# Kernel tuning notes

Hardware: AMD Instinct MI355X
Metric: run time of the kernel (lower is better)

## Reference

```python
import jax, jax.numpy as jnp
import numpy as np

HEADS = 16
DIM_HEAD = 64
QUERY_DIM = 1024
INNER = HEADS * DIM_HEAD


def setup_inputs() -> dict:
    key = jax.random.key(0)
    ks = jax.random.split(key, 6)
    b, n = 4, 2048
    s = 0.02
    return {
        "x": jax.random.normal(ks[0], (b, n, QUERY_DIM), dtype=jnp.float32),
        "Wq": jax.random.normal(ks[1], (QUERY_DIM, INNER), dtype=jnp.float32) * s,
        "Wk": jax.random.normal(ks[2], (QUERY_DIM, INNER), dtype=jnp.float32) * s,
        "Wv": jax.random.normal(ks[3], (QUERY_DIM, INNER), dtype=jnp.float32) * s,
        "Wo": jax.random.normal(ks[4], (INNER, QUERY_DIM), dtype=jnp.float32) * s,
        "bo": jax.random.normal(ks[5], (QUERY_DIM,), dtype=jnp.float32) * s,
    }


def reference(x, Wq, Wk, Wv, Wo, bo):
    b, n, _ = x.shape
    scale = DIM_HEAD ** (-0.5)
    # project and split heads: [b, n, inner] -> [b, h, n, d]
    def split(t):
        return t.reshape(b, n, HEADS, DIM_HEAD).transpose(0, 2, 1, 3)
    q = split(x @ Wq)
    k = split(x @ Wk)
    v = split(x @ Wv)
    sim = jnp.einsum('bhid,bhjd->bhij', q, k) * scale  # [b, h, n, n]
    attn = jax.nn.softmax(sim, axis=-1)
    out = jnp.einsum('bhij,bhjd->bhid', attn, v)  # [b, h, n, d]
    out = out.transpose(0, 2, 1, 3).reshape(b, n, INNER)
    return out @ Wo + bo
```

## Files before the change

### kernel.cpp

```cpp
#include <hip/hip_runtime.h>

typedef __attribute__((ext_vector_type(8))) short bf16x8;
typedef __attribute__((ext_vector_type(4))) float f32x4;
typedef __attribute__((ext_vector_type(16))) float f32x16;
typedef __attribute__((ext_vector_type(2))) unsigned u32x2;

__device__ __forceinline__ unsigned short f2b(float f) {
  union { float f; unsigned u; } x; x.f = f;
  unsigned r = x.u + 0x7fffu + ((x.u >> 16) & 1u);
  return (unsigned short)(r >> 16);
}

__device__ __forceinline__ int cvt_pk_bf16(float lo, float hi) {
  int r;
  asm("v_cvt_pk_bf16_f32 %0, %1, %2" : "=v"(r) : "v"(lo), "v"(hi));
  return r;
}

__device__ __forceinline__ float exp2_fast(float x) {
#if __has_builtin(__builtin_amdgcn_exp2f)
  return __builtin_amdgcn_exp2f(x);
#else
  return __expf(x * 0.69314718055994531f);
#endif
}

__device__ __forceinline__ void gl_lds16(const unsigned short* g, unsigned short* l) {
  __builtin_amdgcn_global_load_lds(
      (const __attribute__((address_space(1))) unsigned int*)(unsigned long long)g,
      (__attribute__((address_space(3))) unsigned int*)(unsigned)(unsigned long long)l,
      16, 0, 0);
}

#define MFMA(a, b, c) __builtin_amdgcn_mfma_f32_16x16x32_bf16((a), (b), (c), 0, 0, 0)
#define MFMA32(a, b, c) __builtin_amdgcn_mfma_f32_32x32x16_bf16((a), (b), (c), 0, 0, 0)

__global__ __launch_bounds__(256) void prep(const float* __restrict__ x, unsigned short* __restrict__ xb,
                                            const float* __restrict__ wq, const float* __restrict__ wk,
                                            const float* __restrict__ wv, const float* __restrict__ wo,
                                            unsigned short* __restrict__ tq, unsigned short* __restrict__ tk,
                                            unsigned short* __restrict__ tv, unsigned short* __restrict__ to_) {
  int lin = blockIdx.x;
  int t = threadIdx.x;
  if (lin < 8192) {
    int i = (lin * 256 + t) * 4;
    float4 v = *(const float4*)(x + i);
    ushort4 o;
    o.x = f2b(v.x); o.y = f2b(v.y); o.z = f2b(v.z); o.w = f2b(v.w);
    *(ushort4*)(xb + i) = o;
    return;
  }
  int blk = lin - 8192;
  int z = blk >> 8;
  int rem = blk & 255;
  int by = rem >> 4, bx = rem & 15;
  const float* W = (z == 0) ? wq : (z == 1) ? wk : (z == 2) ? wv : wo;
  unsigned short* T = (z == 0) ? tq : (z == 1) ? tk : (z == 2) ? tv : to_;
  float scale = (z == 0) ? 0.125f * 1.4426950408889634f : 1.0f;
  __shared__ float tile[64][65];
  int tr = by * 64, tc = bx * 64;
  int col = t & 63, r0 = (t >> 6) * 16;
#pragma unroll
  for (int r = 0; r < 16; r++)
    tile[r0 + r][col] = W[(long)(tr + r0 + r) * 1024 + tc + col];
  __syncthreads();
  int k = t & 63, n0 = (t >> 6) * 16;
#pragma unroll
  for (int n = 0; n < 16; n++)
    T[(long)(tc + n0 + n) * 1024 + tr + k] = f2b(tile[k][n0 + n] * scale);
}

__device__ __forceinline__ void gemm_core_256x128(const unsigned short* __restrict__ A,
                                                  const unsigned short* __restrict__ BT,
                                                  int m0, int n0,
                                                  unsigned short* As, unsigned short* Bs,
                                                  f32x4 acc[8][2]) {
  const int t = threadIdx.x;
  const int lane = t & 63;
  const int wid = t >> 6;
  const int wr = wid >> 2, wc = wid & 3;
  const int c = lane & 15, g = lane >> 4;

#define SA(hk, kt_, db)                                                                \
  {                                                                                    \
    _Pragma("unroll")                                                                  \
    for (int j = 0; j < 2; j++) {                                                      \
      int idx = j * 512 + t;                                                           \
      int row = idx >> 2, pl = idx & 3;                                                \
      int sc = (hk) * 4 + (pl ^ ((row >> 1) & 3));                                     \
      gl_lds16(A + (long)(m0 + row) * 1024 + (kt_) * 64 + sc * 8,                      \
               As + (db) * 16384 + (hk) * 8192 + idx * 8);                             \
    }                                                                                  \
  }
#define SB(hk, kt_, db)                                                                \
  {                                                                                    \
    int row = t >> 2, pl = t & 3;                                                      \
    int sc = (hk) * 4 + (pl ^ ((row >> 1) & 3));                                       \
    gl_lds16(BT + (long)(n0 + row) * 1024 + (kt_) * 64 + sc * 8,                       \
             Bs + (db) * 8192 + (hk) * 4096 + t * 8);                                  \
  }

#define RD_B(dstv, ks, buf)                                                            \
  {                                                                                    \
    _Pragma("unroll")                                                                  \
    for (int ni = 0; ni < 2; ni++) {                                                   \
      int row = wc * 32 + ni * 16 + c;                                                 \
      dstv[ni] = *(const bf16x8*)(Bs + (buf) * 8192 + (ks) * 4096 + row * 32 +         \
                                  ((g ^ ((row >> 1) & 3)) * 8));                       \
    }                                                                                  \
  }
#define RD_A(dstv, ks, qm, buf)                                                        \
  {                                                                                    \
    _Pragma("unroll")                                                                  \
    for (int i = 0; i < 4; i++) {                                                      \
      int row = wr * 128 + ((qm) * 4 + i) * 16 + c;                                    \
      dstv[i] = *(const bf16x8*)(As + (buf) * 16384 + (ks) * 8192 + row * 32 +         \
                                 ((g ^ ((row >> 1) & 3)) * 8));                        \
    }                                                                                  \
  }
#define DO_MFMA(afv, bfv, qm)                                                          \
  __builtin_amdgcn_s_setprio(1);                                                       \
  _Pragma("unroll")                                                                    \
  for (int i = 0; i < 4; i++)                                                          \
    _Pragma("unroll")                                                                  \
    for (int ni = 0; ni < 2; ni++)                                                     \
      acc[(qm) * 4 + i][ni] = MFMA(afv[i], bfv[ni], acc[(qm) * 4 + i][ni]);            \
  __builtin_amdgcn_s_setprio(0);

#define SYNC(n)                                                                        \
  asm volatile("s_waitcnt vmcnt(" #n ")" ::: "memory");                                \
  __builtin_amdgcn_s_barrier();                                                        \
  __builtin_amdgcn_sched_barrier(0);

  SA(0, 0, 0); SB(0, 0, 0); SA(1, 0, 0); SB(1, 0, 0);

  for (int kt = 0; kt < 16; kt++) {
    int buf = kt & 1, nb = buf ^ 1;
    bf16x8 af[4], bf[2];
    SYNC(3)
    RD_B(bf, 0, buf);
    RD_A(af, 0, 0, buf);
    if (kt < 15) SA(0, kt + 1, nb);
    DO_MFMA(af, bf, 0)
    RD_A(af, 0, 1, buf);
    if (kt < 15) SB(0, kt + 1, nb);
    DO_MFMA(af, bf, 1)
    if (kt < 15) { SYNC(3) } else { SYNC(0) }
    RD_B(bf, 1, buf);
    RD_A(af, 1, 0, buf);
    if (kt < 15) SA(1, kt + 1, nb);
    DO_MFMA(af, bf, 0)
    RD_A(af, 1, 1, buf);
    if (kt < 15) SB(1, kt + 1, nb);
    DO_MFMA(af, bf, 1)
  }
#undef SA
#undef SB
#undef RD_A
#undef RD_B
#undef DO_MFMA
#undef SYNC
}

__global__ __launch_bounds__(512) void gemm_qkv(const unsigned short* __restrict__ xb,
                                                const unsigned short* __restrict__ wtq,
                                                const unsigned short* __restrict__ wtk,
                                                const unsigned short* __restrict__ wtv,
                                                unsigned short* __restrict__ Qw,
                                                unsigned short* __restrict__ Kw,
                                                unsigned short* __restrict__ Vtw) {
  __shared__ unsigned short As[2 * 16384], Bs[2 * 8192];
  int m0 = blockIdx.x * 256;
  int nglob0 = blockIdx.y * 128;
  int which = nglob0 >> 10;
  const unsigned short* BT = (which == 0) ? wtq : (which == 1) ? wtk : wtv;
  int n0 = nglob0 & 1023;
  f32x4 acc[8][2] = {};
  gemm_core_256x128(xb, BT, m0, n0, As, Bs, acc);

  const int t = threadIdx.x;
  const int lane = t & 63, wid = t >> 6;
  const int wr = wid >> 2, wc = wid & 3;
  const int c = lane & 15, g = lane >> 4;
  int b = m0 >> 11;
  int ibase = m0 & 2047;
#pragma unroll
  for (int mi = 0; mi < 8; mi++) {
    int irow0 = ibase + wr * 128 + mi * 16 + g * 4;
#pragma unroll
    for (int ni = 0; ni < 2; ni++) {
      int nl = n0 + wc * 32 + ni * 16 + c;
      int h = nl >> 6, d = nl & 63;
      if (which == 2) {
        ushort4 pk;
        pk.x = f2b(acc[mi][ni][0]); pk.y = f2b(acc[mi][ni][1]);
        pk.z = f2b(acc[mi][ni][2]); pk.w = f2b(acc[mi][ni][3]);
        *(ushort4*)(Vtw + ((long)(b * 16 + h) * 64 + d) * 2048 + irow0) = pk;
      } else {
        unsigned short* dst = (which == 0) ? Qw : Kw;
#pragma unroll
        for (int r = 0; r < 4; r++)
          dst[((long)(b * 16 + h) * 2048 + irow0 + r) * 64 + d] = f2b(acc[mi][ni][r]);
      }
    }
  }
}

__global__ __launch_bounds__(512) void gemm_out(const unsigned short* __restrict__ Ao,
                                                const unsigned short* __restrict__ wto,
                                                const float* __restrict__ bias,
                                                float* __restrict__ out) {
  __shared__ unsigned short As[2 * 16384], Bs[2 * 8192];
  int m0 = blockIdx.x * 256;
  int n0 = blockIdx.y * 128;
  f32x4 acc[8][2] = {};
  gemm_core_256x128(Ao, wto, m0, n0, As, Bs, acc);

  const int t = threadIdx.x;
  const int lane = t & 63, wid = t >> 6;
  const int wr = wid >> 2, wc = wid & 3;
  const int c = lane & 15, g = lane >> 4;
#pragma unroll
  for (int mi = 0; mi < 8; mi++)
#pragma unroll
    for (int ni = 0; ni < 2; ni++) {
      int col = n0 + wc * 32 + ni * 16 + c;
      float bv = bias[col];
#pragma unroll
      for (int r = 0; r < 4; r++) {
        int row = m0 + wr * 128 + mi * 16 + g * 4 + r;
        out[(long)row * 1024 + col] = acc[mi][ni][r] + bv;
      }
    }
}

__global__ __launch_bounds__(512) void attn(const unsigned short* __restrict__ Qw,
                                            const unsigned short* __restrict__ Kw,
                                            const unsigned short* __restrict__ Vtw,
                                            unsigned short* __restrict__ Ow) {
  int ib = blockIdx.y * 8 + blockIdx.x;
  int xcd = ib & 7, j = ib >> 3;
  int bh = xcd * 8 + (j >> 3);
  int qt = j & 7;
  int t = threadIdx.x;
  int lane = t & 63, wid = t >> 6;
  int c5 = lane & 31, h = lane >> 5;
  __shared__ unsigned short Ks[3][64 * 64];
  __shared__ unsigned short Vs[3][64 * 64];

  const unsigned short* Qp = Qw + ((long)bh * 2048 + qt * 256 + wid * 32 + c5) * 64 + h * 8;
  bf16x8 qf[4];
#pragma unroll
  for (int dK = 0; dK < 4; dK++) qf[dK] = *(const bf16x8*)(Qp + dK * 16);

  f32x16 oacc0 = {}, oacc1 = {};
  float ls0 = 0.f, ls1 = 0.f, ls2 = 0.f, ls3 = 0.f;

  const unsigned short* Kbase = Kw + (long)bh * 2048 * 64;
  const unsigned short* Vbase = Vtw + (long)bh * 64 * 2048;

#define STAGE(jt_, buf_)                                                              \
  {                                                                                   \
    int row = t >> 3, ch = t & 7;                                                     \
    int sw = ch ^ (row & 7);                                                          \
    gl_lds16(Kbase + (long)((jt_) * 64 + row) * 64 + sw * 8, &Ks[buf_][t * 8]);       \
    gl_lds16(Vbase + (long)row * 2048 + (jt_) * 64 + sw * 8, &Vs[buf_][t * 8]);       \
  }

  STAGE(0, 0);
  STAGE(1, 1);

  union FR { int i[4]; bf16x8 v; };

  for (int jt = 0; jt < 32; jt++) {
    int buf = jt % 3;
    if (jt < 31) {
      asm volatile("s_waitcnt vmcnt(2)" ::: "memory");
    } else {
      asm volatile("s_waitcnt vmcnt(0)" ::: "memory");
    }
    __builtin_amdgcn_s_barrier();
    __builtin_amdgcn_sched_barrier(0);
    if (jt + 2 < 32) STAGE(jt + 2, (jt + 2) % 3);

    f32x16 s0 = {}, s1 = {};
#pragma unroll
    for (int dK = 0; dK < 4; dK++) {
      int sw = ((dK * 2 + h) ^ (c5 & 7)) * 8;
      bf16x8 k0 = *(const bf16x8*)(&Ks[buf][c5 * 64 + sw]);
      bf16x8 k1 = *(const bf16x8*)(&Ks[buf][c5 * 64 + sw + 2048]);
      s0 = MFMA32(k0, qf[dK], s0);
      s1 = MFMA32(k1, qf[dK], s1);
    }

    int pk[2][4][2];
#pragma unroll
    for (int q2 = 0; q2 < 4; q2++) {
      float a0 = exp2_fast(s0[q2 * 4 + 0]), a1 = exp2_fast(s0[q2 * 4 + 1]);
      float a2 = exp2_fast(s0[q2 * 4 + 2]), a3 = exp2_fast(s0[q2 * 4 + 3]);
      ls0 += a0 + a1; ls1 += a2 + a3;
      pk[0][q2][0] = cvt_pk_bf16(a0, a1);
      pk[0][q2][1] = cvt_pk_bf16(a2, a3);
      float b0 = exp2_fast(s1[q2 * 4 + 0]), b1 = exp2_fast(s1[q2 * 4 + 1]);
      float b2 = exp2_fast(s1[q2 * 4 + 2]), b3 = exp2_fast(s1[q2 * 4 + 3]);
      ls2 += b0 + b1; ls3 += b2 + b3;
      pk[1][q2][0] = cvt_pk_bf16(b0, b1);
      pk[1][q2][1] = cvt_pk_bf16(b2, b3);
    }

#pragma unroll
    for (int kblk = 0; kblk < 4; kblk++) {
      int kvb = kblk >> 1, e2c = (kblk & 1) * 2;
      u32x2 p0 = __builtin_amdgcn_permlane32_swap((unsigned)pk[kvb][e2c][0],
                                                  (unsigned)pk[kvb][e2c + 1][0], false, false);
      u32x2 p1 = __builtin_amdgcn_permlane32_swap((unsigned)pk[kvb][e2c][1],
                                                  (unsigned)pk[kvb][e2c + 1][1], false, false);
      FR fr;
      fr.i[0] = (int)p0[0];
      fr.i[1] = (int)p1[0];
      fr.i[2] = (int)p0[1];
      fr.i[3] = (int)p1[1];
      int sw = ((kblk * 2 + h) ^ (c5 & 7)) * 8;
      bf16x8 v0 = *(const bf16x8*)(&Vs[buf][c5 * 64 + sw]);
      bf16x8 v1 = *(const bf16x8*)(&Vs[buf][c5 * 64 + sw + 2048]);
      oacc0 = MFMA32(v0, fr.v, oacc0);
      oacc1 = MFMA32(v1, fr.v, oacc1);
    }
  }
#undef STAGE

  float lsum = ls0 + ls1 + ls2 + ls3;
  lsum += __shfl_xor(lsum, 32);
  float inv = 1.0f / lsum;
  int b = bh >> 4, hh = bh & 15;
  long row = (long)b * 2048 + qt * 256 + wid * 32 + c5;
  unsigned short* orow = Ow + row * 1024 + hh * 64;
#pragma unroll
  for (int dblk = 0; dblk < 2; dblk++) {
#pragma unroll
    for (int q2 = 0; q2 < 4; q2++) {
      float o0 = (dblk ? oacc1 : oacc0)[q2 * 4 + 0] * inv;
      float o1 = (dblk ? oacc1 : oacc0)[q2 * 4 + 1] * inv;
      float o2 = (dblk ? oacc1 : oacc0)[q2 * 4 + 2] * inv;
      float o3 = (dblk ? oacc1 : oacc0)[q2 * 4 + 3] * inv;
      ushort4 pkv;
      pkv.x = f2b(o0); pkv.y = f2b(o1); pkv.z = f2b(o2); pkv.w = f2b(o3);
      *(ushort4*)(orow + dblk * 32 + q2 * 8 + h * 4) = pkv;
    }
  }
}

extern "C" void kernel_launch(void* const* d_in, const int* in_sizes, int n_in,
                              void* d_out, int out_size, void* d_ws, size_t ws_size,
                              hipStream_t stream) {
  const float* x  = (const float*)d_in[0];
  const float* Wq = (const float*)d_in[1];
  const float* Wk = (const float*)d_in[2];
  const float* Wv = (const float*)d_in[3];
  const float* Wo = (const float*)d_in[4];
  const float* bo = (const float*)d_in[5];
  float* out = (float*)d_out;

  char* ws = (char*)d_ws;
  unsigned short* xb  = (unsigned short*)(ws);
  unsigned short* wtq = (unsigned short*)(ws + 16777216);
  unsigned short* wtk = (unsigned short*)(ws + 16777216 + 2097152);
  unsigned short* wtv = (unsigned short*)(ws + 16777216 + 2 * 2097152);
  unsigned short* wto = (unsigned short*)(ws + 16777216 + 3 * 2097152);
  unsigned short* Qw  = (unsigned short*)(ws + 25165824);
  unsigned short* Kw  = (unsigned short*)(ws + 25165824 + 16777216);
  unsigned short* Vtw = (unsigned short*)(ws + 25165824 + 2 * 16777216);
  unsigned short* Aow = xb;

  prep<<<9216, 256, 0, stream>>>(x, xb, Wq, Wk, Wv, Wo, wtq, wtk, wtv, wto);
  gemm_qkv<<<dim3(32, 24), 512, 0, stream>>>(xb, wtq, wtk, wtv, Qw, Kw, Vtw);
  attn<<<dim3(8, 64), 512, 0, stream>>>(Qw, Kw, Vtw, Aow);
  gemm_out<<<dim3(32, 8), 512, 0, stream>>>(Aow, wto, bo, out);
}
```

Measured before the change: 166.2 us.

## Double query rows per wave in attention, halving block size to 256 threads

The attention kernel now runs 4 waves per block instead of 8, and each wave handles 64 query rows (two 32-row groups) rather than 32. Each K/V fragment read from LDS therefore feeds twice as many MFMAs, and each thread issues two loads per tensor per stage to fill the same 64x64 tiles. This cuts LDS read traffic per FLOP, at the cost of more accumulator registers per wave and fewer waves per block to hide latency.

```diff
diff --git a/kernel.cpp b/kernel.cpp
--- a/kernel.cpp
+++ b/kernel.cpp
@@ -234,7 +234,7 @@
     }
 }
 
-__global__ __launch_bounds__(512) void attn(const unsigned short* __restrict__ Qw,
+__global__ __launch_bounds__(256) void attn(const unsigned short* __restrict__ Qw,
                                             const unsigned short* __restrict__ Kw,
                                             const unsigned short* __restrict__ Vtw,
                                             unsigned short* __restrict__ Ow) {
@@ -248,13 +248,16 @@
   __shared__ unsigned short Ks[3][64 * 64];
   __shared__ unsigned short Vs[3][64 * 64];
 
-  const unsigned short* Qp = Qw + ((long)bh * 2048 + qt * 256 + wid * 32 + c5) * 64 + h * 8;
-  bf16x8 qf[4];
-#pragma unroll
-  for (int dK = 0; dK < 4; dK++) qf[dK] = *(const bf16x8*)(Qp + dK * 16);
-
-  f32x16 oacc0 = {}, oacc1 = {};
-  float ls0 = 0.f, ls1 = 0.f, ls2 = 0.f, ls3 = 0.f;
+  const unsigned short* Qp = Qw + ((long)bh * 2048 + qt * 256 + wid * 64 + c5) * 64 + h * 8;
+  bf16x8 qf0[4], qf1[4];
+#pragma unroll
+  for (int dK = 0; dK < 4; dK++) {
+    qf0[dK] = *(const bf16x8*)(Qp + dK * 16);
+    qf1[dK] = *(const bf16x8*)(Qp + 32 * 64 + dK * 16);
+  }
+
+  f32x16 oacc00 = {}, oacc01 = {}, oacc10 = {}, oacc11 = {};
+  float ls0a = 0.f, ls0b = 0.f, ls1a = 0.f, ls1b = 0.f;
 
   const unsigned short* Kbase = Kw + (long)bh * 2048 * 64;
   const unsigned short* Vbase = Vtw + (long)bh * 64 * 2048;
@@ -264,7 +267,11 @@
     int row = t >> 3, ch = t & 7;                                                     \
     int sw = ch ^ (row & 7);                                                          \
     gl_lds16(Kbase + (long)((jt_) * 64 + row) * 64 + sw * 8, &Ks[buf_][t * 8]);       \
+    gl_lds16(Kbase + (long)((jt_) * 64 + row + 32) * 64 + sw * 8,                     \
+             &Ks[buf_][(t + 256) * 8]);                                               \
     gl_lds16(Vbase + (long)row * 2048 + (jt_) * 64 + sw * 8, &Vs[buf_][t * 8]);       \
+    gl_lds16(Vbase + (long)(row + 32) * 2048 + (jt_) * 64 + sw * 8,                   \
+             &Vs[buf_][(t + 256) * 8]);                                               \
   }
 
   STAGE(0, 0);
@@ -275,7 +282,7 @@
   for (int jt = 0; jt < 32; jt++) {
     int buf = jt % 3;
     if (jt < 31) {
-      asm volatile("s_waitcnt vmcnt(2)" ::: "memory");
+      asm volatile("s_waitcnt vmcnt(4)" ::: "memory");
     } else {
       asm volatile("s_waitcnt vmcnt(0)" ::: "memory");
     }
@@ -283,69 +290,97 @@
     __builtin_amdgcn_sched_barrier(0);
     if (jt + 2 < 32) STAGE(jt + 2, (jt + 2) % 3);
 
-    f32x16 s0 = {}, s1 = {};
+    f32x16 s00 = {}, s01 = {}, s10 = {}, s11 = {};
 #pragma unroll
     for (int dK = 0; dK < 4; dK++) {
       int sw = ((dK * 2 + h) ^ (c5 & 7)) * 8;
       bf16x8 k0 = *(const bf16x8*)(&Ks[buf][c5 * 64 + sw]);
       bf16x8 k1 = *(const bf16x8*)(&Ks[buf][c5 * 64 + sw + 2048]);
-      s0 = MFMA32(k0, qf[dK], s0);
-      s1 = MFMA32(k1, qf[dK], s1);
-    }
-
-    int pk[2][4][2];
+      s00 = MFMA32(k0, qf0[dK], s00);
+      s01 = MFMA32(k1, qf0[dK], s01);
+      s10 = MFMA32(k0, qf1[dK], s10);
+      s11 = MFMA32(k1, qf1[dK], s11);
+    }
+
+    int pk0[2][4][2], pk1[2][4][2];
 #pragma unroll
     for (int q2 = 0; q2 < 4; q2++) {
-      float a0 = exp2_fast(s0[q2 * 4 + 0]), a1 = exp2_fast(s0[q2 * 4 + 1]);
-      float a2 = exp2_fast(s0[q2 * 4 + 2]), a3 = exp2_fast(s0[q2 * 4 + 3]);
-      ls0 += a0 + a1; ls1 += a2 + a3;
-      pk[0][q2][0] = cvt_pk_bf16(a0, a1);
-      pk[0][q2][1] = cvt_pk_bf16(a2, a3);
-      float b0 = exp2_fast(s1[q2 * 4 + 0]), b1 = exp2_fast(s1[q2 * 4 + 1]);
-      float b2 = exp2_fast(s1[q2 * 4 + 2]), b3 = exp2_fast(s1[q2 * 4 + 3]);
-      ls2 += b0 + b1; ls3 += b2 + b3;
-      pk[1][q2][0] = cvt_pk_bf16(b0, b1);
-      pk[1][q2][1] = cvt_pk_bf16(b2, b3);
+      float a0 = exp2_fast(s00[q2 * 4 + 0]), a1 = exp2_fast(s00[q2 * 4 + 1]);
+      float a2 = exp2_fast(s00[q2 * 4 + 2]), a3 = exp2_fast(s00[q2 * 4 + 3]);
+      ls0a += a0 + a1 + a2 + a3;
+      pk0[0][q2][0] = cvt_pk_bf16(a0, a1);
+      pk0[0][q2][1] = cvt_pk_bf16(a2, a3);
+      float b0 = exp2_fast(s01[q2 * 4 + 0]), b1 = exp2_fast(s01[q2 * 4 + 1]);
+      float b2 = exp2_fast(s01[q2 * 4 + 2]), b3 = exp2_fast(s01[q2 * 4 + 3]);
+      ls0b += b0 + b1 + b2 + b3;
+      pk0[1][q2][0] = cvt_pk_bf16(b0, b1);
+      pk0[1][q2][1] = cvt_pk_bf16(b2, b3);
+      float c0 = exp2_fast(s10[q2 * 4 + 0]), c1 = exp2_fast(s10[q2 * 4 + 1]);
+      float c2 = exp2_fast(s10[q2 * 4 + 2]), c3 = exp2_fast(s10[q2 * 4 + 3]);
+      ls1a += c0 + c1 + c2 + c3;
+      pk1[0][q2][0] = cvt_pk_bf16(c0, c1);
+      pk1[0][q2][1] = cvt_pk_bf16(c2, c3);
+      float d0 = exp2_fast(s11[q2 * 4 + 0]), d1 = exp2_fast(s11[q2 * 4 + 1]);
+      float d2 = exp2_fast(s11[q2 * 4 + 2]), d3 = exp2_fast(s11[q2 * 4 + 3]);
+      ls1b += d0 + d1 + d2 + d3;
+      pk1[1][q2][0] = cvt_pk_bf16(d0, d1);
+      pk1[1][q2][1] = cvt_pk_bf16(d2, d3);
     }
 
 #pragma unroll
     for (int kblk = 0; kblk < 4; kblk++) {
       int kvb = kblk >> 1, e2c = (kblk & 1) * 2;
-      u32x2 p0 = __builtin_amdgcn_permlane32_swap((unsigned)pk[kvb][e2c][0],
-                                                  (unsigned)pk[kvb][e2c + 1][0], false, false);
-      u32x2 p1 = __builtin_amdgcn_permlane32_swap((unsigned)pk[kvb][e2c][1],
-                                                  (unsigned)pk[kvb][e2c + 1][1], false, false);
-      FR fr;
-      fr.i[0] = (int)p0[0];
-      fr.i[1] = (int)p1[0];
-      fr.i[2] = (int)p0[1];
-      fr.i[3] = (int)p1[1];
       int sw = ((kblk * 2 + h) ^ (c5 & 7)) * 8;
       bf16x8 v0 = *(const bf16x8*)(&Vs[buf][c5 * 64 + sw]);
       bf16x8 v1 = *(const bf16x8*)(&Vs[buf][c5 * 64 + sw + 2048]);
-      oacc0 = MFMA32(v0, fr.v, oacc0);
-      oacc1 = MFMA32(v1, fr.v, oacc1);
+      {
+        u32x2 p0 = __builtin_amdgcn_permlane32_swap((unsigned)pk0[kvb][e2c][0],
+                                                    (unsigned)pk0[kvb][e2c + 1][0], false, false);
+        u32x2 p1 = __builtin_amdgcn_permlane32_swap((unsigned)pk0[kvb][e2c][1],
+                                                    (unsigned)pk0[kvb][e2c + 1][1], false, false);
+        FR fr;
+        fr.i[0] = (int)p0[0]; fr.i[1] = (int)p1[0];
+        fr.i[2] = (int)p0[1]; fr.i[3] = (int)p1[1];
+        oacc00 = MFMA32(v0, fr.v, oacc00);
+        oacc01 = MFMA32(v1, fr.v, oacc01);
+      }
+      {
+        u32x2 p0 = __builtin_amdgcn_permlane32_swap((unsigned)pk1[kvb][e2c][0],
+                                                    (unsigned)pk1[kvb][e2c + 1][0], false, false);
+        u32x2 p1 = __builtin_amdgcn_permlane32_swap((unsigned)pk1[kvb][e2c][1],
+                                                    (unsigned)pk1[kvb][e2c + 1][1], false, false);
+        FR fr;
+        fr.i[0] = (int)p0[0]; fr.i[1] = (int)p1[0];
+        fr.i[2] = (int)p0[1]; fr.i[3] = (int)p1[1];
+        oacc10 = MFMA32(v0, fr.v, oacc10);
+        oacc11 = MFMA32(v1, fr.v, oacc11);
+      }
     }
   }
 #undef STAGE
 
-  float lsum = ls0 + ls1 + ls2 + ls3;
-  lsum += __shfl_xor(lsum, 32);
-  float inv = 1.0f / lsum;
   int b = bh >> 4, hh = bh & 15;
-  long row = (long)b * 2048 + qt * 256 + wid * 32 + c5;
-  unsigned short* orow = Ow + row * 1024 + hh * 64;
-#pragma unroll
-  for (int dblk = 0; dblk < 2; dblk++) {
-#pragma unroll
-    for (int q2 = 0; q2 < 4; q2++) {
-      float o0 = (dblk ? oacc1 : oacc0)[q2 * 4 + 0] * inv;
-      float o1 = (dblk ? oacc1 : oacc0)[q2 * 4 + 1] * inv;
-      float o2 = (dblk ? oacc1 : oacc0)[q2 * 4 + 2] * inv;
-      float o3 = (dblk ? oacc1 : oacc0)[q2 * 4 + 3] * inv;
-      ushort4 pkv;
-      pkv.x = f2b(o0); pkv.y = f2b(o1); pkv.z = f2b(o2); pkv.w = f2b(o3);
-      *(ushort4*)(orow + dblk * 32 + q2 * 8 + h * 4) = pkv;
+#pragma unroll
+  for (int grp = 0; grp < 2; grp++) {
+    float lsum = grp ? (ls1a + ls1b) : (ls0a + ls0b);
+    lsum += __shfl_xor(lsum, 32);
+    float inv = 1.0f / lsum;
+    long row = (long)b * 2048 + qt * 256 + wid * 64 + grp * 32 + c5;
+    unsigned short* orow = Ow + row * 1024 + hh * 64;
+    const f32x16& oa = grp ? oacc10 : oacc00;
+    const f32x16& ob = grp ? oacc11 : oacc01;
+#pragma unroll
+    for (int dblk = 0; dblk < 2; dblk++) {
+#pragma unroll
+      for (int q2 = 0; q2 < 4; q2++) {
+        float o0 = (dblk ? ob : oa)[q2 * 4 + 0] * inv;
+        float o1 = (dblk ? ob : oa)[q2 * 4 + 1] * inv;
+        float o2 = (dblk ? ob : oa)[q2 * 4 + 2] * inv;
+        float o3 = (dblk ? ob : oa)[q2 * 4 + 3] * inv;
+        ushort4 pkv;
+        pkv.x = f2b(o0); pkv.y = f2b(o1); pkv.z = f2b(o2); pkv.w = f2b(o3);
+        *(ushort4*)(orow + dblk * 32 + q2 * 8 + h * 4) = pkv;
+      }
     }
   }
 }
@@ -374,6 +409,6 @@
 
   prep<<<9216, 256, 0, stream>>>(x, xb, Wq, Wk, Wv, Wo, wtq, wtk, wtv, wto);
   gemm_qkv<<<dim3(32, 24), 512, 0, stream>>>(xb, wtq, wtk, wtv, Qw, Kw, Vtw);
-  attn<<<dim3(8, 64), 512, 0, stream>>>(Qw, Kw, Vtw, Aow);
+  attn<<<dim3(8, 64), 256, 0, stream>>>(Qw, Kw, Vtw, Aow);
   gemm_out<<<dim3(32, 8), 512, 0, stream>>>(Aow, wto, bo, out);
 }
```

Result: slower. 177.7 us (+6.9%).
